# Performance work log

Measured on AMD Instinct MI355X. Metric: run time of the kernel, lower is better.

The kernel has to match this reference:

```python
import jax, jax.numpy as jnp
import numpy as np

T, B, IN, H, F, OUT = 2048, 32, 256, 512, 2048, 256


def setup_inputs() -> dict:
    key = jax.random.key(0)
    ks = jax.random.split(key, 9)
    s_in = 1.0 / np.sqrt(IN)
    s_h = 1.0 / np.sqrt(H)
    s_f = 1.0 / np.sqrt(F)
    return {
        "x": jax.random.normal(ks[0], (T, B, IN), dtype=jnp.float32),
        "Wg": jax.random.uniform(ks[1], (H, IN), jnp.float32, -s_in, s_in),
        "bg": jax.random.uniform(ks[2], (H,), jnp.float32, -s_in, s_in),
        "Wi": jax.random.uniform(ks[3], (H, IN), jnp.float32, -s_in, s_in),
        "bi": jax.random.uniform(ks[4], (H,), jnp.float32, -s_in, s_in),
        "W1": jax.random.uniform(ks[5], (F, H), jnp.float32, -s_h, s_h),
        "b1": jax.random.uniform(ks[6], (F,), jnp.float32, -s_h, s_h),
        "W2": jax.random.uniform(ks[7], (OUT, F), jnp.float32, -s_f, s_f),
        "b2": jax.random.uniform(ks[8], (OUT,), jnp.float32, -s_f, s_f),
    }


def _gilr_scan(a, b):
    # h_t = a_t * h_{t-1} + b_t with h_0 = 0  ->  parallel associative scan over time
    def combine(c1, c2):
        a1, b1 = c1
        a2, b2 = c2
        return (a1 * a2, b1 * a2 + b2)
    _, h = jax.lax.associative_scan(combine, (a, b), axis=0)
    return h


def reference(x, Wg, bg, Wi, bi, W1, b1, W2, b2):
    # x: (T, B, IN)
    g = jax.nn.sigmoid(jnp.einsum("tbi,hi->tbh", x, Wg) + bg)  # (T,B,H)
    i = jnp.tanh(jnp.einsum("tbi,hi->tbh", x, Wi) + bi)        # (T,B,H)
    h = _gilr_scan(g, (1.0 - g) * i)                             # (T,B,H)
    z = jax.nn.gelu(jnp.einsum("tbh,fh->tbf", h, W1) + b1, approximate=False)
    out = jnp.einsum("tbf,of->tbo", z, W2) + b2                  # (T,B,OUT)
    return out
```

## Files before the change

### kernel.cpp

```cpp
#include <hip/hip_runtime.h>
#include <hip/hip_fp16.h>
#include <math.h>


#define IN_DIM 256
#define H_DIM 512
#define F_DIM 2048
#define OUT_DIM 256

typedef _Float16 f16;
typedef _Float16 f16x8 __attribute__((ext_vector_type(8)));
typedef float f32x4 __attribute__((ext_vector_type(4)));

#define AS3(p) ((__attribute__((address_space(3))) void*)(p))
#define AS1(p) ((const __attribute__((address_space(1))) void*)(p))
#define MFMA16(d, x, y) d = __builtin_amdgcn_mfma_f32_16x16x32_f16(x, y, d, 0, 0, 0)


__global__ void cvt_kernel(const float* __restrict__ in, f16* __restrict__ out, int n8) {
  int i = blockIdx.x * blockDim.x + threadIdx.x;
  if (i >= n8) return;
  const float4* p = (const float4*)in + (size_t)i * 2;
  float4 a = p[0], b = p[1];
  f16x8 o = { (f16)a.x, (f16)a.y, (f16)a.z, (f16)a.w,
              (f16)b.x, (f16)b.y, (f16)b.z, (f16)b.w };
  *((f16x8*)out + i) = o;
}

__global__ void bias_cat_kernel(const float* __restrict__ bg, const float* __restrict__ bi,
                                float* __restrict__ bgi) {
  int t = threadIdx.x;
  bgi[t] = (t < 512) ? bg[t] : bi[t - 512];
}

__device__ __forceinline__ float sigmoid_fast(float v) {
  return __builtin_amdgcn_rcpf(1.0f + __expf(-v));
}
__device__ __forceinline__ float tanh_fast(float v) {
  return 1.0f - 2.0f * __builtin_amdgcn_rcpf(__expf(2.0f * v) + 1.0f);
}
__device__ __forceinline__ float gelu_fast(float v) {
  float u = v * v;
  float y = v * fmaf(0.0713548353f, u, 1.59576912161f);
  return v * __builtin_amdgcn_rcpf(1.0f + __expf(-y));
}


__global__ __launch_bounds__(256, 2) void gemm1_k(
    const float* __restrict__ X, const f16* __restrict__ Bw,
    const float* __restrict__ bias, f16* __restrict__ Cout) {
  constexpr int LDB = 256, LDC = 1024, NT = 8;
  __shared__ f16 lds[24576];
  const int tid = threadIdx.x, wid = tid >> 6, lane = tid & 63;
  const int r = lane & 15;
  const int bid = blockIdx.x;
  const int m0 = ((bid & 7) * 32 + (bid >> 6)) * 256;
  const int n0 = ((bid >> 3) & 7) * 128;
  const int wr = (wid >> 1) * 128, wc = (wid & 1) * 64;

  int aoff[4];
#pragma unroll
  for (int q = 0; q < 4; ++q) {
    int s = wid * 256 + q * 64 + lane;
    int row = s >> 2, g = (s & 3) ^ ((row >> 1) & 3);
    aoff[q] = (m0 + row) * IN_DIM + g * 8;
  }
  const f16* srcB[2];
#pragma unroll
  for (int q = 0; q < 2; ++q) {
    int s = wid * 128 + q * 64 + lane;
    int row = s >> 2, g = (s & 3) ^ ((row >> 1) & 3);
    srcB[q] = Bw + (size_t)(n0 + row) * LDB + g * 8;
  }

  float4 sa[4][2];
  auto loadA = [&](int kt) {
#pragma unroll
    for (int q = 0; q < 4; ++q) {
      const float4* p = (const float4*)(X + (size_t)aoff[q] + kt * 32);
      sa[q][0] = p[0]; sa[q][1] = p[1];
    }
  };
  auto writeA = [&](int buf) {
#pragma unroll
    for (int q = 0; q < 4; ++q) {
      float4 a = sa[q][0], b = sa[q][1];
      f16x8 o = { (f16)a.x, (f16)a.y, (f16)a.z, (f16)a.w,
                  (f16)b.x, (f16)b.y, (f16)b.z, (f16)b.w };
      *(f16x8*)(lds + buf * 8192 + wid * 2048 + q * 512 + lane * 8) = o;
    }
  };
  auto stageB = [&](int buf, int kt) {
#pragma unroll
    for (int q = 0; q < 2; ++q)
      __builtin_amdgcn_global_load_lds(AS1(srcB[q] + kt * 32),
          AS3(lds + 16384 + buf * 4096 + wid * 1024 + q * 512), 16, 0, 0);
  };

  const int xorc = (((lane >> 4) ^ ((r >> 1) & 3)) << 3);
  f32x4 acc[8][4] = {};
  loadA(0); writeA(0); stageB(0, 0);
  for (int kt = 0; kt < NT; ++kt) {
    const int cur = kt & 1, nb = cur ^ 1;
    __syncthreads();
    if (kt + 1 < NT) { loadA(kt + 1); stageB(nb, kt + 1); }
    f16x8 af[8], bf[4];
#pragma unroll
    for (int mi = 0; mi < 8; ++mi)
      af[mi] = *(const f16x8*)(lds + cur * 8192 + (wr + mi * 16 + r) * 32 + xorc);
#pragma unroll
    for (int ni = 0; ni < 4; ++ni)
      bf[ni] = *(const f16x8*)(lds + 16384 + cur * 4096 + (wc + ni * 16 + r) * 32 + xorc);
#pragma unroll
    for (int mi = 0; mi < 8; ++mi)
#pragma unroll
      for (int ni = 0; ni < 4; ++ni)
        MFMA16(acc[mi][ni], af[mi], bf[ni]);
    if (kt + 1 < NT) writeA(nb);
  }

  __syncthreads();
  f16* ep = lds + wid * 4096;
  const int rq = (lane >> 4) * 4;
#pragma unroll
  for (int h = 0; h < 2; ++h) {
#pragma unroll
    for (int mi = 0; mi < 4; ++mi) {
#pragma unroll
      for (int ni = 0; ni < 4; ++ni) {
        int gcol = n0 + wc + ni * 16 + r;
        float bv = bias[gcol];
        bool sig = gcol < 512;
        int cc = ni * 2 + (r >> 3);
#pragma unroll
        for (int j = 0; j < 4; ++j) {
          int lrow = mi * 16 + rq + j;
          float v = acc[h * 4 + mi][ni][j] + bv;
          float av = sig ? sigmoid_fast(v) : tanh_fast(v);
          ep[lrow * 64 + ((cc ^ (lrow & 7)) << 3) + (r & 7)] = (f16)av;
        }
      }
    }
    asm volatile("s_waitcnt lgkmcnt(0)" ::: "memory");
    __builtin_amdgcn_sched_barrier(0);
#pragma unroll
    for (int t = 0; t < 8; ++t) {
      int idx = t * 64 + lane;
      int row = idx >> 3, c = idx & 7;
      f16x8 v = *(const f16x8*)(ep + row * 64 + ((c ^ (row & 7)) << 3));
      *(f16x8*)(Cout + (size_t)(m0 + wr + h * 64 + row) * LDC + n0 + wc + c * 8) = v;
    }
    asm volatile("s_waitcnt lgkmcnt(0)" ::: "memory");
    __builtin_amdgcn_sched_barrier(0);
  }
}


__global__ __launch_bounds__(256, 2) void gemm2_k(
    const f16* __restrict__ A, const f16* __restrict__ Bw,
    const float* __restrict__ bias, f16* __restrict__ Cout) {
  constexpr int LDA = 1024, LDB = 512, LDC = 2048, NT = 16;
  __shared__ f16 lds[24576];
  const int tid = threadIdx.x, wid = tid >> 6, lane = tid & 63;
  const int r = lane & 15;
  const int bid = blockIdx.x;
  const int m0 = ((bid & 7) * 8 + (bid >> 7)) * 256;
  const int n0 = ((bid >> 3) & 15) * 128;
  const int wr = (wid >> 1) * 128, wc = (wid & 1) * 64;

  const f16* srcA[4];
  const f16* srcB[2];
#pragma unroll
  for (int q = 0; q < 4; ++q) {
    int s = wid * 256 + q * 64 + lane;
    int row = s >> 2, g = (s & 3) ^ ((row >> 1) & 3);
    srcA[q] = A + (size_t)(m0 + row) * LDA + g * 8;
  }
#pragma unroll
  for (int q = 0; q < 2; ++q) {
    int s = wid * 128 + q * 64 + lane;
    int row = s >> 2, g = (s & 3) ^ ((row >> 1) & 3);
    srcB[q] = Bw + (size_t)(n0 + row) * LDB + g * 8;
  }
  auto stage = [&](int buf, int kt) {
#pragma unroll
    for (int q = 0; q < 4; ++q)
      __builtin_amdgcn_global_load_lds(AS1(srcA[q] + kt * 32),
          AS3(lds + buf * 8192 + wid * 2048 + q * 512), 16, 0, 0);
#pragma unroll
    for (int q = 0; q < 2; ++q)
      __builtin_amdgcn_global_load_lds(AS1(srcB[q] + kt * 32),
          AS3(lds + 16384 + buf * 4096 + wid * 1024 + q * 512), 16, 0, 0);
  };

  const int xorc = (((lane >> 4) ^ ((r >> 1) & 3)) << 3);
  f32x4 acc[8][4] = {};
  stage(0, 0);
  for (int kt = 0; kt < NT; ++kt) {
    const int cur = kt & 1;
    __syncthreads();
    if (kt + 1 < NT) stage(cur ^ 1, kt + 1);
    f16x8 af[8], bf[4];
#pragma unroll
    for (int mi = 0; mi < 8; ++mi)
      af[mi] = *(const f16x8*)(lds + cur * 8192 + (wr + mi * 16 + r) * 32 + xorc);
#pragma unroll
    for (int ni = 0; ni < 4; ++ni)
      bf[ni] = *(const f16x8*)(lds + 16384 + cur * 4096 + (wc + ni * 16 + r) * 32 + xorc);
#pragma unroll
    for (int mi = 0; mi < 8; ++mi)
#pragma unroll
      for (int ni = 0; ni < 4; ++ni)
        MFMA16(acc[mi][ni], af[mi], bf[ni]);
  }

  __syncthreads();
  f16* ep = lds + wid * 4096;
  const int rq = (lane >> 4) * 4;
#pragma unroll
  for (int h = 0; h < 2; ++h) {
#pragma unroll
    for (int mi = 0; mi < 4; ++mi) {
#pragma unroll
      for (int ni = 0; ni < 4; ++ni) {
        float bv = bias[n0 + wc + ni * 16 + r];
        int cc = ni * 2 + (r >> 3);
#pragma unroll
        for (int j = 0; j < 4; ++j) {
          int lrow = mi * 16 + rq + j;
          float v = gelu_fast(acc[h * 4 + mi][ni][j] + bv);
          ep[lrow * 64 + ((cc ^ (lrow & 7)) << 3) + (r & 7)] = (f16)v;
        }
      }
    }
    asm volatile("s_waitcnt lgkmcnt(0)" ::: "memory");
    __builtin_amdgcn_sched_barrier(0);
#pragma unroll
    for (int t = 0; t < 8; ++t) {
      int idx = t * 64 + lane;
      int row = idx >> 3, c = idx & 7;
      f16x8 v = *(const f16x8*)(ep + row * 64 + ((c ^ (row & 7)) << 3));
      *(f16x8*)(Cout + (size_t)(m0 + wr + h * 64 + row) * LDC + n0 + wc + c * 8) = v;
    }
    asm volatile("s_waitcnt lgkmcnt(0)" ::: "memory");
    __builtin_amdgcn_sched_barrier(0);
  }
}


__global__ __launch_bounds__(256, 2) void gemm3_k(
    const f16* __restrict__ A, const f16* __restrict__ Bw,
    const float* __restrict__ bias, float* __restrict__ Cout) {
  constexpr int LDA = 2048, LDB = 2048, LDC = 256, NT = 32;
  __shared__ f16 lds[2][2][128][64];
  const int tid = threadIdx.x, wid = tid >> 6, lane = tid & 63;
  const int bid = blockIdx.x;
  const int m0 = ((bid & 7) * 16 + (bid >> 4)) * 128;
  const int n0 = ((bid >> 3) & 1) * 128;
  const int wr = (wid >> 1) * 64, wc = (wid & 1) * 64;

  auto stage = [&](int buf, int kt) {
    const f16* ga = A + (size_t)m0 * LDA + kt * 64;
    const f16* gb = Bw + (size_t)n0 * LDB + kt * 64;
    f16* la = &lds[buf][0][0][0];
    f16* lb = &lds[buf][1][0][0];
#pragma unroll
    for (int q = 0; q < 4; ++q) {
      int seg = (wid << 2) + q;
      int s = seg * 64 + lane;
      int row = s >> 3, col = (s & 7) << 3;
      __builtin_amdgcn_global_load_lds(AS1(ga + (size_t)row * LDA + col),
                                       AS3(la + seg * 512), 16, 0, 0);
      __builtin_amdgcn_global_load_lds(AS1(gb + (size_t)row * LDB + col),
                                       AS3(lb + seg * 512), 16, 0, 0);
    }
  };

  f32x4 acc[4][4] = {};
  stage(0, 0);
  for (int kt = 0; kt < NT; ++kt) {
    __syncthreads();
    if (kt + 1 < NT) stage((kt + 1) & 1, kt + 1);
    f16(*At)[64] = lds[kt & 1][0];
    f16(*Bt)[64] = lds[kt & 1][1];
    const int r = lane & 15, cg = (lane >> 4) << 3;
#pragma unroll
    for (int kk = 0; kk < 2; ++kk) {
      f16x8 af[4], bf[4];
#pragma unroll
      for (int i = 0; i < 4; ++i)
        af[i] = *(const f16x8*)&At[wr + i * 16 + r][kk * 32 + cg];
#pragma unroll
      for (int i = 0; i < 4; ++i)
        bf[i] = *(const f16x8*)&Bt[wc + i * 16 + r][kk * 32 + cg];
#pragma unroll
      for (int mi = 0; mi < 4; ++mi)
#pragma unroll
        for (int ni = 0; ni < 4; ++ni)
          MFMA16(acc[mi][ni], af[mi], bf[ni]);
    }
  }
  const int r = lane & 15, rq = (lane >> 4) * 4;
#pragma unroll
  for (int ni = 0; ni < 4; ++ni) {
    int col = n0 + wc + ni * 16 + r;
    float bv = bias[col];
#pragma unroll
    for (int mi = 0; mi < 4; ++mi) {
#pragma unroll
      for (int j = 0; j < 4; ++j) {
        int row = m0 + wr + mi * 16 + rq + j;
        Cout[(size_t)row * LDC + col] = acc[mi][ni][j] + bv;
      }
    }
  }
}


#define NCH 16384
#define NCHUNK 32
#define CLEN 64

__global__ void scan_p1(const f16* __restrict__ ab, float* __restrict__ cA,
                        float* __restrict__ cH) {
  int ch = blockIdx.x * 256 + threadIdx.x;
  int c = blockIdx.y;
  const f16* pg = ab + (size_t)(c * CLEN) * 32768 + (ch >> 9) * 1024 + (ch & 511);
  const f16* pi = pg + 512;
  float A = 1.f, Hl = 0.f;
  for (int t = 0; t < CLEN; ++t) {
    float g = (float)pg[0];
    float ii = (float)pi[0];
    Hl = fmaf(g, Hl - ii, ii);
    A *= g;
    pg += 32768; pi += 32768;
  }
  cA[c * NCH + ch] = A;
  cH[c * NCH + ch] = Hl;
}

__global__ void scan_p2(const float* __restrict__ cA, const float* __restrict__ cH,
                        float* __restrict__ st) {
  int ch = blockIdx.x * 256 + threadIdx.x;
  float h0 = 0.f;
  for (int c = 0; c < NCHUNK; ++c) {
    st[c * NCH + ch] = h0;
    h0 = cA[c * NCH + ch] * h0 + cH[c * NCH + ch];
  }
}

__global__ void scan_p3(f16* __restrict__ ab, const float* __restrict__ st) {
  int ch = blockIdx.x * 256 + threadIdx.x;
  int c = blockIdx.y;
  f16* pg = ab + (size_t)(c * CLEN) * 32768 + (ch >> 9) * 1024 + (ch & 511);
  const f16* pi = pg + 512;
  float hv = st[c * NCH + ch];
  for (int t = 0; t < CLEN; ++t) {
    float g = (float)pg[0];
    float ii = (float)pi[0];
    hv = fmaf(g, hv - ii, ii);
    pg[0] = (f16)hv;
    pg += 32768; pi += 32768;
  }
}


extern "C" void kernel_launch(void* const* d_in, const int* in_sizes, int n_in,
                              void* d_out, int out_size, void* d_ws, size_t ws_size,
                              hipStream_t stream) {
  const float* x  = (const float*)d_in[0];
  const float* Wg = (const float*)d_in[1];
  const float* bg = (const float*)d_in[2];
  const float* Wi = (const float*)d_in[3];
  const float* bi = (const float*)d_in[4];
  const float* W1 = (const float*)d_in[5];
  const float* b1 = (const float*)d_in[6];
  const float* W2 = (const float*)d_in[7];
  const float* b2 = (const float*)d_in[8];
  float* out = (float*)d_out;

  char* ws = (char*)d_ws;
  f16*   wgi16 = (f16*)(ws + 0);
  f16*   w116  = (f16*)(ws + 524288);
  f16*   w216  = (f16*)(ws + 2621440);
  float* bgi   = (float*)(ws + 3670016);
  f16*   ab16  = (f16*)(ws + 37748736);
  float* cA    = (float*)(ws + 171966464);
  float* cH    = (float*)(ws + 174063616);
  float* st    = (float*)(ws + 176160768);
  f16*   z16   = (f16*)(ws + 178257920);
  if (ws_size < 245366784) return;

  cvt_kernel<<<64, 256, 0, stream>>>(Wg, wgi16, 16384);
  cvt_kernel<<<64, 256, 0, stream>>>(Wi, wgi16 + 131072, 16384);
  cvt_kernel<<<512, 256, 0, stream>>>(W1, w116, 131072);
  cvt_kernel<<<256, 256, 0, stream>>>(W2, w216, 65536);
  bias_cat_kernel<<<1, 1024, 0, stream>>>(bg, bi, bgi);

  gemm1_k<<<2048, 256, 0, stream>>>(x, wgi16, bgi, ab16);

  scan_p1<<<dim3(64, NCHUNK), 256, 0, stream>>>(ab16, cA, cH);
  scan_p2<<<64, 256, 0, stream>>>(cA, cH, st);
  scan_p3<<<dim3(64, NCHUNK), 256, 0, stream>>>(ab16, st);

  for (int s = 0; s < 4; ++s) {
    const f16* hs = ab16 + (size_t)s * 16384 * 1024;
    gemm2_k<<<1024, 256, 0, stream>>>(hs, w116, b1, z16);
    gemm3_k<<<256, 256, 0, stream>>>(z16, w216, b2, out + (size_t)s * 16384 * 256);
  }
}
```

Baseline: 509.5 us.

## Shrink gemm1/gemm2 tiles to 128x128 and pre-convert x to fp16

Both GEMM kernels drop from 256x128 to 128x128 block tiles with 4x4 MFMA accumulators per wave, and launch bounds rise to 4 blocks per CU with a smaller LDS footprint. The aim is higher occupancy and better latency hiding. gemm1 no longer converts fp32 x to fp16 in registers. A separate cvt_kernel now writes fp16 x to workspace, so gemm1 can stage A with direct global-to-LDS loads like gemm2. The cost is an extra pass over x (read fp32, write fp16), more blocks, and lower operand reuse per tile.

```diff
diff --git a/kernel.cpp b/kernel.cpp
--- a/kernel.cpp
+++ b/kernel.cpp
@@ -46,204 +46,162 @@
 }
 
 
-__global__ __launch_bounds__(256, 2) void gemm1_k(
-    const float* __restrict__ X, const f16* __restrict__ Bw,
+__global__ __launch_bounds__(256, 4) void gemm1_k(
+    const f16* __restrict__ A, const f16* __restrict__ Bw,
     const float* __restrict__ bias, f16* __restrict__ Cout) {
-  constexpr int LDB = 256, LDC = 1024, NT = 8;
-  __shared__ f16 lds[24576];
+  constexpr int LDA = 256, LDB = 256, LDC = 1024, NT = 8;
+  __shared__ f16 lds[2][2][128][32];
   const int tid = threadIdx.x, wid = tid >> 6, lane = tid & 63;
+  const int bid = blockIdx.x;
+  const int m0 = ((bid & 7) * 64 + (bid >> 6)) * 128;
+  const int n0 = ((bid >> 3) & 7) * 128;
+  const int wr = (wid >> 1) * 64, wc = (wid & 1) * 64;
+
+  const f16* srcA[2]; const f16* srcB[2];
+#pragma unroll
+  for (int q = 0; q < 2; ++q) {
+    int s = (wid * 2 + q) * 64 + lane;
+    int row = s >> 2, g = (s & 3) ^ ((row >> 1) & 3);
+    srcA[q] = A + (size_t)(m0 + row) * LDA + g * 8;
+    srcB[q] = Bw + (size_t)(n0 + row) * LDB + g * 8;
+  }
+  auto stage = [&](int buf, int kt) {
+    f16* la = &lds[buf][0][0][0] + (wid * 2) * 512;
+    f16* lb = &lds[buf][1][0][0] + (wid * 2) * 512;
+#pragma unroll
+    for (int q = 0; q < 2; ++q) {
+      __builtin_amdgcn_global_load_lds(AS1(srcA[q] + kt * 32), AS3(la + q * 512), 16, 0, 0);
+      __builtin_amdgcn_global_load_lds(AS1(srcB[q] + kt * 32), AS3(lb + q * 512), 16, 0, 0);
+    }
+  };
   const int r = lane & 15;
-  const int bid = blockIdx.x;
-  const int m0 = ((bid & 7) * 32 + (bid >> 6)) * 256;
-  const int n0 = ((bid >> 3) & 7) * 128;
-  const int wr = (wid >> 1) * 128, wc = (wid & 1) * 64;
-
-  int aoff[4];
-#pragma unroll
-  for (int q = 0; q < 4; ++q) {
-    int s = wid * 256 + q * 64 + lane;
-    int row = s >> 2, g = (s & 3) ^ ((row >> 1) & 3);
-    aoff[q] = (m0 + row) * IN_DIM + g * 8;
-  }
-  const f16* srcB[2];
-#pragma unroll
-  for (int q = 0; q < 2; ++q) {
-    int s = wid * 128 + q * 64 + lane;
-    int row = s >> 2, g = (s & 3) ^ ((row >> 1) & 3);
-    srcB[q] = Bw + (size_t)(n0 + row) * LDB + g * 8;
-  }
-
-  float4 sa[4][2];
-  auto loadA = [&](int kt) {
-#pragma unroll
-    for (int q = 0; q < 4; ++q) {
-      const float4* p = (const float4*)(X + (size_t)aoff[q] + kt * 32);
-      sa[q][0] = p[0]; sa[q][1] = p[1];
-    }
-  };
-  auto writeA = [&](int buf) {
-#pragma unroll
-    for (int q = 0; q < 4; ++q) {
-      float4 a = sa[q][0], b = sa[q][1];
-      f16x8 o = { (f16)a.x, (f16)a.y, (f16)a.z, (f16)a.w,
-                  (f16)b.x, (f16)b.y, (f16)b.z, (f16)b.w };
-      *(f16x8*)(lds + buf * 8192 + wid * 2048 + q * 512 + lane * 8) = o;
-    }
-  };
-  auto stageB = [&](int buf, int kt) {
-#pragma unroll
-    for (int q = 0; q < 2; ++q)
-      __builtin_amdgcn_global_load_lds(AS1(srcB[q] + kt * 32),
-          AS3(lds + 16384 + buf * 4096 + wid * 1024 + q * 512), 16, 0, 0);
-  };
-
-  const int xorc = (((lane >> 4) ^ ((r >> 1) & 3)) << 3);
-  f32x4 acc[8][4] = {};
-  loadA(0); writeA(0); stageB(0, 0);
+  const int cs = (((lane >> 4) ^ ((lane >> 1) & 3)) << 3);
+
+  f32x4 acc[4][4] = {};
+  stage(0, 0);
   for (int kt = 0; kt < NT; ++kt) {
-    const int cur = kt & 1, nb = cur ^ 1;
     __syncthreads();
-    if (kt + 1 < NT) { loadA(kt + 1); stageB(nb, kt + 1); }
-    f16x8 af[8], bf[4];
-#pragma unroll
-    for (int mi = 0; mi < 8; ++mi)
-      af[mi] = *(const f16x8*)(lds + cur * 8192 + (wr + mi * 16 + r) * 32 + xorc);
-#pragma unroll
-    for (int ni = 0; ni < 4; ++ni)
-      bf[ni] = *(const f16x8*)(lds + 16384 + cur * 4096 + (wc + ni * 16 + r) * 32 + xorc);
-#pragma unroll
-    for (int mi = 0; mi < 8; ++mi)
+    if (kt + 1 < NT) stage((kt + 1) & 1, kt + 1);
+    f16(*At)[32] = lds[kt & 1][0];
+    f16(*Bt)[32] = lds[kt & 1][1];
+    f16x8 af[4], bf[4];
+#pragma unroll
+    for (int i = 0; i < 4; ++i) af[i] = *(const f16x8*)&At[wr + i * 16 + r][cs];
+#pragma unroll
+    for (int i = 0; i < 4; ++i) bf[i] = *(const f16x8*)&Bt[wc + i * 16 + r][cs];
+#pragma unroll
+    for (int mi = 0; mi < 4; ++mi)
 #pragma unroll
       for (int ni = 0; ni < 4; ++ni)
         MFMA16(acc[mi][ni], af[mi], bf[ni]);
-    if (kt + 1 < NT) writeA(nb);
   }
 
   __syncthreads();
-  f16* ep = lds + wid * 4096;
+  const bool sig = n0 < 512;
+  f16* ep = &lds[0][0][0][0] + wid * 4096;
   const int rq = (lane >> 4) * 4;
 #pragma unroll
-  for (int h = 0; h < 2; ++h) {
+  for (int ni = 0; ni < 4; ++ni) {
+    float bv = bias[n0 + wc + ni * 16 + r];
+    int cc = ni * 2 + (r >> 3);
 #pragma unroll
     for (int mi = 0; mi < 4; ++mi) {
 #pragma unroll
-      for (int ni = 0; ni < 4; ++ni) {
-        int gcol = n0 + wc + ni * 16 + r;
-        float bv = bias[gcol];
-        bool sig = gcol < 512;
-        int cc = ni * 2 + (r >> 3);
-#pragma unroll
-        for (int j = 0; j < 4; ++j) {
-          int lrow = mi * 16 + rq + j;
-          float v = acc[h * 4 + mi][ni][j] + bv;
-          float av = sig ? sigmoid_fast(v) : tanh_fast(v);
-          ep[lrow * 64 + ((cc ^ (lrow & 7)) << 3) + (r & 7)] = (f16)av;
-        }
+      for (int j = 0; j < 4; ++j) {
+        int lrow = mi * 16 + rq + j;
+        float v = acc[mi][ni][j] + bv;
+        float av = sig ? sigmoid_fast(v) : tanh_fast(v);
+        ep[lrow * 64 + ((cc ^ (lrow & 7)) << 3) + (r & 7)] = (f16)av;
       }
     }
-    asm volatile("s_waitcnt lgkmcnt(0)" ::: "memory");
-    __builtin_amdgcn_sched_barrier(0);
-#pragma unroll
-    for (int t = 0; t < 8; ++t) {
-      int idx = t * 64 + lane;
-      int row = idx >> 3, c = idx & 7;
-      f16x8 v = *(const f16x8*)(ep + row * 64 + ((c ^ (row & 7)) << 3));
-      *(f16x8*)(Cout + (size_t)(m0 + wr + h * 64 + row) * LDC + n0 + wc + c * 8) = v;
-    }
-    asm volatile("s_waitcnt lgkmcnt(0)" ::: "memory");
-    __builtin_amdgcn_sched_barrier(0);
-  }
-}
-
-
-__global__ __launch_bounds__(256, 2) void gemm2_k(
+  }
+  asm volatile("s_waitcnt lgkmcnt(0)" ::: "memory");
+  __builtin_amdgcn_sched_barrier(0);
+#pragma unroll
+  for (int t = 0; t < 8; ++t) {
+    int idx = t * 64 + lane;
+    int row = idx >> 3, c = idx & 7;
+    f16x8 v = *(const f16x8*)(ep + row * 64 + ((c ^ (row & 7)) << 3));
+    *(f16x8*)(Cout + (size_t)(m0 + wr + row) * LDC + n0 + wc + c * 8) = v;
+  }
+}
+
+
+__global__ __launch_bounds__(256, 4) void gemm2_k(
     const f16* __restrict__ A, const f16* __restrict__ Bw,
     const float* __restrict__ bias, f16* __restrict__ Cout) {
   constexpr int LDA = 1024, LDB = 512, LDC = 2048, NT = 16;
-  __shared__ f16 lds[24576];
+  __shared__ f16 lds[2][2][128][32];
   const int tid = threadIdx.x, wid = tid >> 6, lane = tid & 63;
-  const int r = lane & 15;
   const int bid = blockIdx.x;
-  const int m0 = ((bid & 7) * 8 + (bid >> 7)) * 256;
+  const int m0 = ((bid & 7) * 16 + (bid >> 7)) * 128;
   const int n0 = ((bid >> 3) & 15) * 128;
-  const int wr = (wid >> 1) * 128, wc = (wid & 1) * 64;
-
-  const f16* srcA[4];
-  const f16* srcB[2];
-#pragma unroll
-  for (int q = 0; q < 4; ++q) {
-    int s = wid * 256 + q * 64 + lane;
+  const int wr = (wid >> 1) * 64, wc = (wid & 1) * 64;
+
+  const f16* srcA[2]; const f16* srcB[2];
+#pragma unroll
+  for (int q = 0; q < 2; ++q) {
+    int s = (wid * 2 + q) * 64 + lane;
     int row = s >> 2, g = (s & 3) ^ ((row >> 1) & 3);
     srcA[q] = A + (size_t)(m0 + row) * LDA + g * 8;
-  }
-#pragma unroll
-  for (int q = 0; q < 2; ++q) {
-    int s = wid * 128 + q * 64 + lane;
-    int row = s >> 2, g = (s & 3) ^ ((row >> 1) & 3);
     srcB[q] = Bw + (size_t)(n0 + row) * LDB + g * 8;
   }
   auto stage = [&](int buf, int kt) {
-#pragma unroll
-    for (int q = 0; q < 4; ++q)
-      __builtin_amdgcn_global_load_lds(AS1(srcA[q] + kt * 32),
-          AS3(lds + buf * 8192 + wid * 2048 + q * 512), 16, 0, 0);
-#pragma unroll
-    for (int q = 0; q < 2; ++q)
-      __builtin_amdgcn_global_load_lds(AS1(srcB[q] + kt * 32),
-          AS3(lds + 16384 + buf * 4096 + wid * 1024 + q * 512), 16, 0, 0);
+    f16* la = &lds[buf][0][0][0] + (wid * 2) * 512;
+    f16* lb = &lds[buf][1][0][0] + (wid * 2) * 512;
+#pragma unroll
+    for (int q = 0; q < 2; ++q) {
+      __builtin_amdgcn_global_load_lds(AS1(srcA[q] + kt * 32), AS3(la + q * 512), 16, 0, 0);
+      __builtin_amdgcn_global_load_lds(AS1(srcB[q] + kt * 32), AS3(lb + q * 512), 16, 0, 0);
+    }
   };
-
-  const int xorc = (((lane >> 4) ^ ((r >> 1) & 3)) << 3);
-  f32x4 acc[8][4] = {};
+  const int r = lane & 15;
+  const int cs = (((lane >> 4) ^ ((lane >> 1) & 3)) << 3);
+
+  f32x4 acc[4][4] = {};
   stage(0, 0);
   for (int kt = 0; kt < NT; ++kt) {
-    const int cur = kt & 1;
     __syncthreads();
-    if (kt + 1 < NT) stage(cur ^ 1, kt + 1);
-    f16x8 af[8], bf[4];
-#pragma unroll
-    for (int mi = 0; mi < 8; ++mi)
-      af[mi] = *(const f16x8*)(lds + cur * 8192 + (wr + mi * 16 + r) * 32 + xorc);
-#pragma unroll
-    for (int ni = 0; ni < 4; ++ni)
-      bf[ni] = *(const f16x8*)(lds + 16384 + cur * 4096 + (wc + ni * 16 + r) * 32 + xorc);
-#pragma unroll
-    for (int mi = 0; mi < 8; ++mi)
+    if (kt + 1 < NT) stage((kt + 1) & 1, kt + 1);
+    f16(*At)[32] = lds[kt & 1][0];
+    f16(*Bt)[32] = lds[kt & 1][1];
+    f16x8 af[4], bf[4];
+#pragma unroll
+    for (int i = 0; i < 4; ++i) af[i] = *(const f16x8*)&At[wr + i * 16 + r][cs];
+#pragma unroll
+    for (int i = 0; i < 4; ++i) bf[i] = *(const f16x8*)&Bt[wc + i * 16 + r][cs];
+#pragma unroll
+    for (int mi = 0; mi < 4; ++mi)
 #pragma unroll
       for (int ni = 0; ni < 4; ++ni)
         MFMA16(acc[mi][ni], af[mi], bf[ni]);
   }
 
   __syncthreads();
-  f16* ep = lds + wid * 4096;
+  f16* ep = &lds[0][0][0][0] + wid * 4096;
   const int rq = (lane >> 4) * 4;
 #pragma unroll
-  for (int h = 0; h < 2; ++h) {
+  for (int ni = 0; ni < 4; ++ni) {
+    float bv = bias[n0 + wc + ni * 16 + r];
+    int cc = ni * 2 + (r >> 3);
 #pragma unroll
     for (int mi = 0; mi < 4; ++mi) {
 #pragma unroll
-      for (int ni = 0; ni < 4; ++ni) {
-        float bv = bias[n0 + wc + ni * 16 + r];
-        int cc = ni * 2 + (r >> 3);
-#pragma unroll
-        for (int j = 0; j < 4; ++j) {
-          int lrow = mi * 16 + rq + j;
-          float v = gelu_fast(acc[h * 4 + mi][ni][j] + bv);
-          ep[lrow * 64 + ((cc ^ (lrow & 7)) << 3) + (r & 7)] = (f16)v;
-        }
+      for (int j = 0; j < 4; ++j) {
+        int lrow = mi * 16 + rq + j;
+        float v = gelu_fast(acc[mi][ni][j] + bv);
+        ep[lrow * 64 + ((cc ^ (lrow & 7)) << 3) + (r & 7)] = (f16)v;
       }
     }
-    asm volatile("s_waitcnt lgkmcnt(0)" ::: "memory");
-    __builtin_amdgcn_sched_barrier(0);
-#pragma unroll
-    for (int t = 0; t < 8; ++t) {
-      int idx = t * 64 + lane;
-      int row = idx >> 3, c = idx & 7;
-      f16x8 v = *(const f16x8*)(ep + row * 64 + ((c ^ (row & 7)) << 3));
-      *(f16x8*)(Cout + (size_t)(m0 + wr + h * 64 + row) * LDC + n0 + wc + c * 8) = v;
-    }
-    asm volatile("s_waitcnt lgkmcnt(0)" ::: "memory");
-    __builtin_amdgcn_sched_barrier(0);
+  }
+  asm volatile("s_waitcnt lgkmcnt(0)" ::: "memory");
+  __builtin_amdgcn_sched_barrier(0);
+#pragma unroll
+  for (int t = 0; t < 8; ++t) {
+    int idx = t * 64 + lane;
+    int row = idx >> 3, c = idx & 7;
+    f16x8 v = *(const f16x8*)(ep + row * 64 + ((c ^ (row & 7)) << 3));
+    *(f16x8*)(Cout + (size_t)(m0 + wr + row) * LDC + n0 + wc + c * 8) = v;
   }
 }
 
@@ -384,6 +342,7 @@
   f16*   w116  = (f16*)(ws + 524288);
   f16*   w216  = (f16*)(ws + 2621440);
   float* bgi   = (float*)(ws + 3670016);
+  f16*   x16   = (f16*)(ws + 4194304);
   f16*   ab16  = (f16*)(ws + 37748736);
   float* cA    = (float*)(ws + 171966464);
   float* cH    = (float*)(ws + 174063616);
@@ -396,8 +355,9 @@
   cvt_kernel<<<512, 256, 0, stream>>>(W1, w116, 131072);
   cvt_kernel<<<256, 256, 0, stream>>>(W2, w216, 65536);
   bias_cat_kernel<<<1, 1024, 0, stream>>>(bg, bi, bgi);
-
-  gemm1_k<<<2048, 256, 0, stream>>>(x, wgi16, bgi, ab16);
+  cvt_kernel<<<8192, 256, 0, stream>>>(x, x16, 2097152);
+
+  gemm1_k<<<4096, 256, 0, stream>>>(x16, wgi16, bgi, ab16);
 
   scan_p1<<<dim3(64, NCHUNK), 256, 0, stream>>>(ab16, cA, cH);
   scan_p2<<<64, 256, 0, stream>>>(cA, cH, st);
@@ -405,7 +365,7 @@
 
   for (int s = 0; s < 4; ++s) {
     const f16* hs = ab16 + (size_t)s * 16384 * 1024;
-    gemm2_k<<<1024, 256, 0, stream>>>(hs, w116, b1, z16);
+    gemm2_k<<<2048, 256, 0, stream>>>(hs, w116, b1, z16);
     gemm3_k<<<256, 256, 0, stream>>>(z16, w216, b2, out + (size_t)s * 16384 * 256);
   }
 }
```

Result: no change. 516.7 us (+1.4%).

## Pre-convert x to fp16 and stage gemm1 A via direct LDS loads; add K64 gemm2 variant

Applied to the files above, without the earlier changes.

Adds a separate conversion pass that turns x into fp16, so gemm1 can load A with global_load_lds like B instead of doing register loads and in-kernel conversion. The sigmoid/tanh choice in gemm1 becomes a per-block uniform test. It also adds gemm2_kb, a single-buffered variant with a K-tile of 64 and an XOR swizzle over 8 groups, used for the last two of the four gemm2 slices. The extra conversion kernel reads and writes x once more in exchange for a simpler gemm1 main loop. Splitting the slices between two gemm2 variants looks like an A/B experiment.

```diff
diff --git a/kernel.cpp b/kernel.cpp
--- a/kernel.cpp
+++ b/kernel.cpp
@@ -47,153 +47,43 @@
 
 
 __global__ __launch_bounds__(256, 2) void gemm1_k(
-    const float* __restrict__ X, const f16* __restrict__ Bw,
+    const f16* __restrict__ A, const f16* __restrict__ Bw,
     const float* __restrict__ bias, f16* __restrict__ Cout) {
-  constexpr int LDB = 256, LDC = 1024, NT = 8;
+  constexpr int LDA = 256, LDB = 256, LDC = 1024, NT = 8;
   __shared__ f16 lds[24576];
   const int tid = threadIdx.x, wid = tid >> 6, lane = tid & 63;
-  const int r = lane & 15;
+  const int lr = lane & 15;
   const int bid = blockIdx.x;
   const int m0 = ((bid & 7) * 32 + (bid >> 6)) * 256;
   const int n0 = ((bid >> 3) & 7) * 128;
   const int wr = (wid >> 1) * 128, wc = (wid & 1) * 64;
 
-  int aoff[4];
+  const f16* srcA[4];
+  const f16* srcB[2];
 #pragma unroll
   for (int q = 0; q < 4; ++q) {
     int s = wid * 256 + q * 64 + lane;
     int row = s >> 2, g = (s & 3) ^ ((row >> 1) & 3);
-    aoff[q] = (m0 + row) * IN_DIM + g * 8;
-  }
-  const f16* srcB[2];
+    srcA[q] = A + (size_t)(m0 + row) * LDA + g * 8;
+  }
 #pragma unroll
   for (int q = 0; q < 2; ++q) {
     int s = wid * 128 + q * 64 + lane;
     int row = s >> 2, g = (s & 3) ^ ((row >> 1) & 3);
     srcB[q] = Bw + (size_t)(n0 + row) * LDB + g * 8;
   }
-
-  float4 sa[4][2];
-  auto loadA = [&](int kt) {
-#pragma unroll
-    for (int q = 0; q < 4; ++q) {
-      const float4* p = (const float4*)(X + (size_t)aoff[q] + kt * 32);
-      sa[q][0] = p[0]; sa[q][1] = p[1];
-    }
-  };
-  auto writeA = [&](int buf) {
-#pragma unroll
-    for (int q = 0; q < 4; ++q) {
-      float4 a = sa[q][0], b = sa[q][1];
-      f16x8 o = { (f16)a.x, (f16)a.y, (f16)a.z, (f16)a.w,
-                  (f16)b.x, (f16)b.y, (f16)b.z, (f16)b.w };
-      *(f16x8*)(lds + buf * 8192 + wid * 2048 + q * 512 + lane * 8) = o;
-    }
-  };
-  auto stageB = [&](int buf, int kt) {
+  auto stage = [&](int buf, int kt) {
+#pragma unroll
+    for (int q = 0; q < 4; ++q)
+      __builtin_amdgcn_global_load_lds(AS1(srcA[q] + kt * 32),
+          AS3(lds + buf * 8192 + wid * 2048 + q * 512), 16, 0, 0);
 #pragma unroll
     for (int q = 0; q < 2; ++q)
       __builtin_amdgcn_global_load_lds(AS1(srcB[q] + kt * 32),
           AS3(lds + 16384 + buf * 4096 + wid * 1024 + q * 512), 16, 0, 0);
   };
 
-  const int xorc = (((lane >> 4) ^ ((r >> 1) & 3)) << 3);
-  f32x4 acc[8][4] = {};
-  loadA(0); writeA(0); stageB(0, 0);
-  for (int kt = 0; kt < NT; ++kt) {
-    const int cur = kt & 1, nb = cur ^ 1;
-    __syncthreads();
-    if (kt + 1 < NT) { loadA(kt + 1); stageB(nb, kt + 1); }
-    f16x8 af[8], bf[4];
-#pragma unroll
-    for (int mi = 0; mi < 8; ++mi)
-      af[mi] = *(const f16x8*)(lds + cur * 8192 + (wr + mi * 16 + r) * 32 + xorc);
-#pragma unroll
-    for (int ni = 0; ni < 4; ++ni)
-      bf[ni] = *(const f16x8*)(lds + 16384 + cur * 4096 + (wc + ni * 16 + r) * 32 + xorc);
-#pragma unroll
-    for (int mi = 0; mi < 8; ++mi)
-#pragma unroll
-      for (int ni = 0; ni < 4; ++ni)
-        MFMA16(acc[mi][ni], af[mi], bf[ni]);
-    if (kt + 1 < NT) writeA(nb);
-  }
-
-  __syncthreads();
-  f16* ep = lds + wid * 4096;
-  const int rq = (lane >> 4) * 4;
-#pragma unroll
-  for (int h = 0; h < 2; ++h) {
-#pragma unroll
-    for (int mi = 0; mi < 4; ++mi) {
-#pragma unroll
-      for (int ni = 0; ni < 4; ++ni) {
-        int gcol = n0 + wc + ni * 16 + r;
-        float bv = bias[gcol];
-        bool sig = gcol < 512;
-        int cc = ni * 2 + (r >> 3);
-#pragma unroll
-        for (int j = 0; j < 4; ++j) {
-          int lrow = mi * 16 + rq + j;
-          float v = acc[h * 4 + mi][ni][j] + bv;
-          float av = sig ? sigmoid_fast(v) : tanh_fast(v);
-          ep[lrow * 64 + ((cc ^ (lrow & 7)) << 3) + (r & 7)] = (f16)av;
-        }
-      }
-    }
-    asm volatile("s_waitcnt lgkmcnt(0)" ::: "memory");
-    __builtin_amdgcn_sched_barrier(0);
-#pragma unroll
-    for (int t = 0; t < 8; ++t) {
-      int idx = t * 64 + lane;
-      int row = idx >> 3, c = idx & 7;
-      f16x8 v = *(const f16x8*)(ep + row * 64 + ((c ^ (row & 7)) << 3));
-      *(f16x8*)(Cout + (size_t)(m0 + wr + h * 64 + row) * LDC + n0 + wc + c * 8) = v;
-    }
-    asm volatile("s_waitcnt lgkmcnt(0)" ::: "memory");
-    __builtin_amdgcn_sched_barrier(0);
-  }
-}
-
-
-__global__ __launch_bounds__(256, 2) void gemm2_k(
-    const f16* __restrict__ A, const f16* __restrict__ Bw,
-    const float* __restrict__ bias, f16* __restrict__ Cout) {
-  constexpr int LDA = 1024, LDB = 512, LDC = 2048, NT = 16;
-  __shared__ f16 lds[24576];
-  const int tid = threadIdx.x, wid = tid >> 6, lane = tid & 63;
-  const int r = lane & 15;
-  const int bid = blockIdx.x;
-  const int m0 = ((bid & 7) * 8 + (bid >> 7)) * 256;
-  const int n0 = ((bid >> 3) & 15) * 128;
-  const int wr = (wid >> 1) * 128, wc = (wid & 1) * 64;
-
-  const f16* srcA[4];
-  const f16* srcB[2];
-#pragma unroll
-  for (int q = 0; q < 4; ++q) {
-    int s = wid * 256 + q * 64 + lane;
-    int row = s >> 2, g = (s & 3) ^ ((row >> 1) & 3);
-    srcA[q] = A + (size_t)(m0 + row) * LDA + g * 8;
-  }
-#pragma unroll
-  for (int q = 0; q < 2; ++q) {
-    int s = wid * 128 + q * 64 + lane;
-    int row = s >> 2, g = (s & 3) ^ ((row >> 1) & 3);
-    srcB[q] = Bw + (size_t)(n0 + row) * LDB + g * 8;
-  }
-  auto stage = [&](int buf, int kt) {
-#pragma unroll
-    for (int q = 0; q < 4; ++q)
-      __builtin_amdgcn_global_load_lds(AS1(srcA[q] + kt * 32),
-          AS3(lds + buf * 8192 + wid * 2048 + q * 512), 16, 0, 0);
-#pragma unroll
-    for (int q = 0; q < 2; ++q)
-      __builtin_amdgcn_global_load_lds(AS1(srcB[q] + kt * 32),
-          AS3(lds + 16384 + buf * 4096 + wid * 1024 + q * 512), 16, 0, 0);
-  };
-
-  const int xorc = (((lane >> 4) ^ ((r >> 1) & 3)) << 3);
+  const int qsf = (((lane >> 4) ^ ((lr >> 1) & 3)) << 3);
   f32x4 acc[8][4] = {};
   stage(0, 0);
   for (int kt = 0; kt < NT; ++kt) {
@@ -203,10 +93,104 @@
     f16x8 af[8], bf[4];
 #pragma unroll
     for (int mi = 0; mi < 8; ++mi)
-      af[mi] = *(const f16x8*)(lds + cur * 8192 + (wr + mi * 16 + r) * 32 + xorc);
+      af[mi] = *(const f16x8*)(lds + cur * 8192 + (wr + mi * 16 + lr) * 32 + qsf);
 #pragma unroll
     for (int ni = 0; ni < 4; ++ni)
-      bf[ni] = *(const f16x8*)(lds + 16384 + cur * 4096 + (wc + ni * 16 + r) * 32 + xorc);
+      bf[ni] = *(const f16x8*)(lds + 16384 + cur * 4096 + (wc + ni * 16 + lr) * 32 + qsf);
+#pragma unroll
+    for (int mi = 0; mi < 8; ++mi)
+#pragma unroll
+      for (int ni = 0; ni < 4; ++ni)
+        MFMA16(acc[mi][ni], af[mi], bf[ni]);
+  }
+
+  __syncthreads();
+  const bool sig = n0 < 512;
+  f16* ep = lds + wid * 4096;
+  const int rq = (lane >> 4) * 4;
+#pragma unroll
+  for (int h = 0; h < 2; ++h) {
+#pragma unroll
+    for (int mi = 0; mi < 4; ++mi) {
+#pragma unroll
+      for (int ni = 0; ni < 4; ++ni) {
+        float bv = bias[n0 + wc + ni * 16 + lr];
+        int cc = ni * 2 + (lr >> 3);
+#pragma unroll
+        for (int j = 0; j < 4; ++j) {
+          int lrow = mi * 16 + rq + j;
+          float v = acc[h * 4 + mi][ni][j] + bv;
+          float av = sig ? sigmoid_fast(v) : tanh_fast(v);
+          ep[lrow * 64 + ((cc ^ (lrow & 7)) << 3) + (lr & 7)] = (f16)av;
+        }
+      }
+    }
+    asm volatile("s_waitcnt lgkmcnt(0)" ::: "memory");
+    __builtin_amdgcn_sched_barrier(0);
+#pragma unroll
+    for (int t = 0; t < 8; ++t) {
+      int idx = t * 64 + lane;
+      int row = idx >> 3, c = idx & 7;
+      f16x8 v = *(const f16x8*)(ep + row * 64 + ((c ^ (row & 7)) << 3));
+      *(f16x8*)(Cout + (size_t)(m0 + wr + h * 64 + row) * LDC + n0 + wc + c * 8) = v;
+    }
+    asm volatile("s_waitcnt lgkmcnt(0)" ::: "memory");
+    __builtin_amdgcn_sched_barrier(0);
+  }
+}
+
+
+__global__ __launch_bounds__(256, 2) void gemm2_k(
+    const f16* __restrict__ A, const f16* __restrict__ Bw,
+    const float* __restrict__ bias, f16* __restrict__ Cout) {
+  constexpr int LDA = 1024, LDB = 512, LDC = 2048, NT = 16;
+  __shared__ f16 lds[24576];
+  const int tid = threadIdx.x, wid = tid >> 6, lane = tid & 63;
+  const int lr = lane & 15;
+  const int bid = blockIdx.x;
+  const int m0 = ((bid & 7) * 8 + (bid >> 7)) * 256;
+  const int n0 = ((bid >> 3) & 15) * 128;
+  const int wr = (wid >> 1) * 128, wc = (wid & 1) * 64;
+
+  const f16* srcA[4];
+  const f16* srcB[2];
+#pragma unroll
+  for (int q = 0; q < 4; ++q) {
+    int s = wid * 256 + q * 64 + lane;
+    int row = s >> 2, g = (s & 3) ^ ((row >> 1) & 3);
+    srcA[q] = A + (size_t)(m0 + row) * LDA + g * 8;
+  }
+#pragma unroll
+  for (int q = 0; q < 2; ++q) {
+    int s = wid * 128 + q * 64 + lane;
+    int row = s >> 2, g = (s & 3) ^ ((row >> 1) & 3);
+    srcB[q] = Bw + (size_t)(n0 + row) * LDB + g * 8;
+  }
+  auto stage = [&](int buf, int kt) {
+#pragma unroll
+    for (int q = 0; q < 4; ++q)
+      __builtin_amdgcn_global_load_lds(AS1(srcA[q] + kt * 32),
+          AS3(lds + buf * 8192 + wid * 2048 + q * 512), 16, 0, 0);
+#pragma unroll
+    for (int q = 0; q < 2; ++q)
+      __builtin_amdgcn_global_load_lds(AS1(srcB[q] + kt * 32),
+          AS3(lds + 16384 + buf * 4096 + wid * 1024 + q * 512), 16, 0, 0);
+  };
+
+  const int qsf = (((lane >> 4) ^ ((lr >> 1) & 3)) << 3);
+  f32x4 acc[8][4] = {};
+  stage(0, 0);
+  for (int kt = 0; kt < NT; ++kt) {
+    const int cur = kt & 1;
+    __syncthreads();
+    if (kt + 1 < NT) stage(cur ^ 1, kt + 1);
+    f16x8 af[8], bf[4];
+#pragma unroll
+    for (int mi = 0; mi < 8; ++mi)
+      af[mi] = *(const f16x8*)(lds + cur * 8192 + (wr + mi * 16 + lr) * 32 + qsf);
+#pragma unroll
+    for (int ni = 0; ni < 4; ++ni)
+      bf[ni] = *(const f16x8*)(lds + 16384 + cur * 4096 + (wc + ni * 16 + lr) * 32 + qsf);
 #pragma unroll
     for (int mi = 0; mi < 8; ++mi)
 #pragma unroll
@@ -223,13 +207,108 @@
     for (int mi = 0; mi < 4; ++mi) {
 #pragma unroll
       for (int ni = 0; ni < 4; ++ni) {
-        float bv = bias[n0 + wc + ni * 16 + r];
-        int cc = ni * 2 + (r >> 3);
+        float bv = bias[n0 + wc + ni * 16 + lr];
+        int cc = ni * 2 + (lr >> 3);
 #pragma unroll
         for (int j = 0; j < 4; ++j) {
           int lrow = mi * 16 + rq + j;
           float v = gelu_fast(acc[h * 4 + mi][ni][j] + bv);
-          ep[lrow * 64 + ((cc ^ (lrow & 7)) << 3) + (r & 7)] = (f16)v;
+          ep[lrow * 64 + ((cc ^ (lrow & 7)) << 3) + (lr & 7)] = (f16)v;
+        }
+      }
+    }
+    asm volatile("s_waitcnt lgkmcnt(0)" ::: "memory");
+    __builtin_amdgcn_sched_barrier(0);
+#pragma unroll
+    for (int t = 0; t < 8; ++t) {
+      int idx = t * 64 + lane;
+      int row = idx >> 3, c = idx & 7;
+      f16x8 v = *(const f16x8*)(ep + row * 64 + ((c ^ (row & 7)) << 3));
+      *(f16x8*)(Cout + (size_t)(m0 + wr + h * 64 + row) * LDC + n0 + wc + c * 8) = v;
+    }
+    asm volatile("s_waitcnt lgkmcnt(0)" ::: "memory");
+    __builtin_amdgcn_sched_barrier(0);
+  }
+}
+
+
+__global__ __launch_bounds__(256, 2) void gemm2_kb(
+    const f16* __restrict__ A, const f16* __restrict__ Bw,
+    const float* __restrict__ bias, f16* __restrict__ Cout) {
+  constexpr int LDA = 1024, LDB = 512, LDC = 2048, NT = 8;
+  __shared__ f16 lds[24576];
+  const int tid = threadIdx.x, wid = tid >> 6, lane = tid & 63;
+  const int lr = lane & 15;
+  const int bid = blockIdx.x;
+  const int m0 = ((bid & 7) * 8 + (bid >> 7)) * 256;
+  const int n0 = ((bid >> 3) & 15) * 128;
+  const int wr = (wid >> 1) * 128, wc = (wid & 1) * 64;
+
+  const f16* srcA[8];
+  const f16* srcB[4];
+#pragma unroll
+  for (int q = 0; q < 8; ++q) {
+    int s = wid * 512 + q * 64 + lane;
+    int row = s >> 3, g = (s & 7) ^ (row & 7);
+    srcA[q] = A + (size_t)(m0 + row) * LDA + g * 8;
+  }
+#pragma unroll
+  for (int q = 0; q < 4; ++q) {
+    int s = wid * 256 + q * 64 + lane;
+    int row = s >> 3, g = (s & 7) ^ (row & 7);
+    srcB[q] = Bw + (size_t)(n0 + row) * LDB + g * 8;
+  }
+  auto stage = [&](int kt) {
+#pragma unroll
+    for (int q = 0; q < 8; ++q)
+      __builtin_amdgcn_global_load_lds(AS1(srcA[q] + kt * 64),
+          AS3(lds + wid * 4096 + q * 512), 16, 0, 0);
+#pragma unroll
+    for (int q = 0; q < 4; ++q)
+      __builtin_amdgcn_global_load_lds(AS1(srcB[q] + kt * 64),
+          AS3(lds + 16384 + wid * 2048 + q * 512), 16, 0, 0);
+  };
+
+  const int qs0 = (((lane >> 4) ^ (lr & 7)) << 3);
+  const int qs1 = (((4 + (lane >> 4)) ^ (lr & 7)) << 3);
+  f32x4 acc[8][4] = {};
+  for (int kt = 0; kt < NT; ++kt) {
+    stage(kt);
+    __syncthreads();
+#pragma unroll
+    for (int kk = 0; kk < 2; ++kk) {
+      const int qs = kk ? qs1 : qs0;
+      f16x8 af[8], bf[4];
+#pragma unroll
+      for (int mi = 0; mi < 8; ++mi)
+        af[mi] = *(const f16x8*)(lds + (wr + mi * 16 + lr) * 64 + qs);
+#pragma unroll
+      for (int ni = 0; ni < 4; ++ni)
+        bf[ni] = *(const f16x8*)(lds + 16384 + (wc + ni * 16 + lr) * 64 + qs);
+#pragma unroll
+      for (int mi = 0; mi < 8; ++mi)
+#pragma unroll
+        for (int ni = 0; ni < 4; ++ni)
+          MFMA16(acc[mi][ni], af[mi], bf[ni]);
+    }
+    __syncthreads();
+  }
+
+  f16* ep = lds + wid * 4096;
+  const int rq = (lane >> 4) * 4;
+#pragma unroll
+  for (int h = 0; h < 2; ++h) {
+#pragma unroll
+    for (int mi = 0; mi < 4; ++mi) {
+#pragma unroll
+      for (int ni = 0; ni < 4; ++ni) {
+        float bv = bias[n0 + wc + ni * 16 + lr];
+        int cc = ni * 2 + (lr >> 3);
+#pragma unroll
+        for (int j = 0; j < 4; ++j) {
+          int lrow = mi * 16 + rq + j;
+          float v = gelu_fast(acc[h * 4 + mi][ni][j] + bv);
+          ep[lrow * 64 + ((cc ^ (lrow & 7)) << 3) + (lr & 7)] = (f16)v;
         }
       }
     }
@@ -384,6 +463,7 @@
   f16*   w116  = (f16*)(ws + 524288);
   f16*   w216  = (f16*)(ws + 2621440);
   float* bgi   = (float*)(ws + 3670016);
+  f16*   x16   = (f16*)(ws + 4194304);
   f16*   ab16  = (f16*)(ws + 37748736);
   float* cA    = (float*)(ws + 171966464);
   float* cH    = (float*)(ws + 174063616);
@@ -396,8 +476,9 @@
   cvt_kernel<<<512, 256, 0, stream>>>(W1, w116, 131072);
   cvt_kernel<<<256, 256, 0, stream>>>(W2, w216, 65536);
   bias_cat_kernel<<<1, 1024, 0, stream>>>(bg, bi, bgi);
-
-  gemm1_k<<<2048, 256, 0, stream>>>(x, wgi16, bgi, ab16);
+  cvt_kernel<<<8192, 256, 0, stream>>>(x, x16, 2097152);
+
+  gemm1_k<<<2048, 256, 0, stream>>>(x16, wgi16, bgi, ab16);
 
   scan_p1<<<dim3(64, NCHUNK), 256, 0, stream>>>(ab16, cA, cH);
   scan_p2<<<64, 256, 0, stream>>>(cA, cH, st);
@@ -405,7 +486,10 @@
 
   for (int s = 0; s < 4; ++s) {
     const f16* hs = ab16 + (size_t)s * 16384 * 1024;
-    gemm2_k<<<1024, 256, 0, stream>>>(hs, w116, b1, z16);
+    if (s < 2)
+      gemm2_k<<<1024, 256, 0, stream>>>(hs, w116, b1, z16);
+    else
+      gemm2_kb<<<1024, 256, 0, stream>>>(hs, w116, b1, z16);
     gemm3_k<<<256, 256, 0, stream>>>(z16, w216, b2, out + (size_t)s * 16384 * 256);
   }
 }
```

Measured after the change: 497.7 us. 2.3% less time.
